# Kernel optimization log

Measured on AMD Instinct MI355X. Metric: run time of the kernel, lower is better.

The kernel has to match this reference:

```python
import jax, jax.numpy as jnp
import numpy as np
from jax import lax

WH = WW = 8          # window size
HEADS = 4

def _rel_index(Wh, Ww):
    # Swin-style static relative position index (N, N) with N = Wh*Ww
    coords = np.stack(np.meshgrid(np.arange(Wh), np.arange(Ww), indexing='ij')).reshape(2, -1)
    rel = coords[:, :, None] - coords[:, None, :]
    rel[0] += Wh - 1
    rel[1] += Ww - 1
    return jnp.asarray(rel[0] * (2 * Ww - 1) + rel[1], dtype=jnp.int32)

REL_IDX = _rel_index(WH, WW)  # (64, 64)

def _rep_pad1_detach(x):
    # ReplicationPad2dNaive(pad=1, detach=True): border copies carry no gradient
    xp = jnp.pad(lax.stop_gradient(x), ((0, 0), (0, 0), (1, 1), (1, 1)), mode='edge')
    return xp.at[:, :, 1:-1, 1:-1].set(x)

def setup_inputs() -> dict:
    key = jax.random.key(0)
    ks = jax.random.split(key, 6)
    B, C, H, W = 8, 192, 192, 192
    mid = 2 * C  # mlp_ratio=2
    s = 0.05
    return {
        'x': jax.random.normal(ks[0], (B, C, H, W), jnp.float32),
        'qkv_w': jax.random.normal(ks[1], (3 * C, C), jnp.float32) * s,
        'qkv_b': jnp.zeros((3 * C,), jnp.float32),
        'proj_w': jax.random.normal(ks[2], (C, C), jnp.float32) * s,
        'proj_b': jnp.zeros((C,), jnp.float32),
        'bias_table': jax.random.normal(ks[3], ((2 * WH - 1) * (2 * WW - 1),), jnp.float32) * s,
        'w1_w': jax.random.normal(ks[4], (mid, C), jnp.float32) * s,
        'w1_b': jnp.zeros((mid,), jnp.float32),
        'w2_w': jax.random.normal(ks[5], (C, mid // 2, 3, 3), jnp.float32) * s,
        'w2_b': jnp.zeros((C,), jnp.float32),
    }

def reference(x, qkv_w, qkv_b, proj_w, proj_b, bias_table, w1_w, w1_b, w2_w, w2_b):
    B, C, H, W = x.shape
    nh, nw = H // WH, W // WW
    N = WH * WW
    d = C // HEADS
    # ---- window partition: (B, C, H, W) -> (B*nWin, N, C) ----
    xw = x.reshape(B, C, nh, WH, nw, WW).transpose(0, 2, 4, 3, 5, 1).reshape(-1, N, C)
    # ---- qkv projection ----
    qkv = xw @ qkv_w.T + qkv_b                              # (Bn, N, 3C)
    qkv = qkv.reshape(-1, N, 3, HEADS, d).transpose(2, 0, 3, 1, 4)
    q, k, v = qkv[0], qkv[1], qkv[2]                        # (Bn, heads, N, d)
    # ---- attention with relative position bias ----
    bias = bias_table[REL_IDX]                              # (N, N)
    scores = jnp.einsum('bhnd,bhmd->bhnm', q, k) / jnp.sqrt(jnp.asarray(d, x.dtype))
    attn = jax.nn.softmax(scores + bias, axis=-1)
    out = jnp.einsum('bhnm,bhmd->bhnd', attn, v)            # (Bn, heads, N, d)
    out = out.transpose(0, 2, 1, 3).reshape(-1, N, C) @ proj_w.T + proj_b
    # ---- reverse window partition ----
    x1 = out.reshape(B, nh, nw, WH, WW, C).transpose(0, 5, 1, 3, 2, 4).reshape(B, C, H, W)
    x = x + x1
    # ---- GLU conv MLP residual branch ----
    h = jnp.einsum('bchw,oc->bohw', x, w1_w) + w1_b[:, None, None]  # 1x1 conv
    a, b = jnp.split(h, 2, axis=1)
    g = a * jax.nn.sigmoid(b)                               # GLU
    g = _rep_pad1_detach(g)
    y = lax.conv_general_dilated(g, w2_w, (1, 1), 'VALID',
                                 dimension_numbers=('NCHW', 'OIHW', 'NCHW'))
    y = y + w2_b[:, None, None]
    y = jnp.where(y >= 0, y, 0.2 * y)                       # leaky_relu(0.2)
    return x + y
```

## Files before the change

### kernel.cpp

```cpp
#include <hip/hip_runtime.h>
#include <hip/hip_bf16.h>

#define HWSZ (192*192)

typedef __attribute__((ext_vector_type(8))) short short8v;
typedef __attribute__((ext_vector_type(4))) float f32x4;

#define WG_N  331776
#define WQ2_N 110592
#define PW2_N 36864
#define W1_N  73728
#define WBYTES ((size_t)2*(WG_N+WQ2_N+PW2_N+W1_N))

__global__ __launch_bounds__(256)
void prep_weights(const float* __restrict__ w2_w, const float* __restrict__ qkv_w,
                  const float* __restrict__ proj_w, const float* __restrict__ w1_w,
                  __hip_bfloat16* __restrict__ wg, __hip_bfloat16* __restrict__ wq,
                  __hip_bfloat16* __restrict__ pw, __hip_bfloat16* __restrict__ w1b)
{
    int i = blockIdx.x*256 + threadIdx.x;
    if (i < WG_N) {
        int tap = i / 36864; int r = i - tap*36864;
        int oc = r / 192;    int c = r - oc*192;
        wg[i] = __float2bfloat16(w2_w[((size_t)oc*192 + c)*9 + tap]);
    } else if (i < WG_N + WQ2_N) {
        int j = i - WG_N;  wq[j] = __float2bfloat16(qkv_w[j]);
    } else if (i < WG_N + WQ2_N + PW2_N) {
        int j = i - WG_N - WQ2_N;  pw[j] = __float2bfloat16(proj_w[j]);
    } else if (i < WG_N + WQ2_N + PW2_N + W1_N) {
        int j = i - WG_N - WQ2_N - PW2_N;  w1b[j] = __float2bfloat16(w1_w[j]);
    }
}

__global__ __launch_bounds__(256, 2)
void wac_fused(const float* __restrict__ x,
               const __hip_bfloat16* __restrict__ wq, const float* __restrict__ qkv_b,
               const __hip_bfloat16* __restrict__ pw, const float* __restrict__ proj_b,
               const __hip_bfloat16* __restrict__ w1b, const float* __restrict__ w1_b,
               const float* __restrict__ bias_tab,
               __hip_bfloat16* __restrict__ g_ws, float* __restrict__ out)
{
    __shared__ __align__(16) __hip_bfloat16 Xs[64][200];
    __shared__ __align__(16) __hip_bfloat16 Os[64][200];
    __shared__ __align__(16) __hip_bfloat16 scr[4][2304];
    __shared__ __align__(16) __hip_bfloat16 bias_bf[64][66];

    const int tid = threadIdx.x;
    const int wid = (blockIdx.x & 7)*576 + (blockIdx.x >> 3);
    const int img = wid / 576;
    const int wr  = wid - img*576;
    const int wi  = wr / 24;
    const int wj  = wr - wi*24;

    const float* xb = x + (size_t)img*192*HWSZ + (size_t)(wi*8)*192 + wj*8;
    for (int i = tid; i < 12288; i += 256) {
        int c = i >> 6, t = i & 63;
        Xs[t][c] = __float2bfloat16(xb[(size_t)c*HWSZ + (t>>3)*192 + (t&7)]);
    }
    for (int i = tid; i < 4096; i += 256) {
        int tq = i >> 6, tk = i & 63;
        bias_bf[tq][tk] = __float2bfloat16(
            bias_tab[((tq>>3)-(tk>>3)+7)*15 + ((tq&7)-(tk&7)+7)]);
    }
    __syncthreads();

    const int lane = tid & 63;
    const int wv   = tid >> 6;
    const int lx   = lane & 15;
    const int kg   = lane >> 4;
    __hip_bfloat16* S = scr[wv];
    const short8v z8 = {0,0,0,0,0,0,0,0};
    const float scale = 0.14433756729740643f;

    short8v qAf[4][2], kBf[4][2], vBf[3][2];
    {
        f32x4 qa[9][4];
        #pragma unroll
        for (int j9=0;j9<9;j9++)
            #pragma unroll
            for (int n=0;n<4;n++) qa[j9][n] = (f32x4){0.f,0.f,0.f,0.f};

        #pragma unroll
        for (int kc=0; kc<6; ++kc) {
            short8v bfX[4];
            #pragma unroll
            for (int n=0;n<4;n++)
                bfX[n] = *(const short8v*)&Xs[n*16+lx][kc*32+kg*8];
            #pragma unroll
            for (int j9=0; j9<9; ++j9) {
                const int reg = j9/3, mm = j9 - reg*3;
                short8v af = *(const short8v*)
                    &wq[(size_t)(reg*192 + wv*48 + mm*16 + lx)*192 + kc*32 + kg*8];
                #pragma unroll
                for (int n=0;n<4;n++)
                    qa[j9][n] = __builtin_amdgcn_mfma_f32_16x16x32_bf16(
                                    af, bfX[n], qa[j9][n], 0,0,0);
            }
        }

        #pragma unroll
        for (int reg=0; reg<2; ++reg) {
            const int jrow0 = reg*192 + wv*48;
            float b4[3][4];
            #pragma unroll
            for (int mm=0;mm<3;mm++)
                #pragma unroll
                for (int r=0;r<4;r++) b4[mm][r] = qkv_b[jrow0 + mm*16 + kg*4 + r];
            #pragma unroll
            for (int hp=0; hp<2; ++hp) {
                #pragma unroll
                for (int mm=0;mm<3;mm++)
                    #pragma unroll
                    for (int nl=0;nl<2;nl++) {
                        union { ushort4 u; __hip_bfloat16 e[4]; } pk;
                        #pragma unroll
                        for (int r=0;r<4;r++)
                            pk.e[r] = __float2bfloat16(qa[reg*3+mm][hp*2+nl][r] + b4[mm][r]);
                        *(ushort4*)&S[(nl*16+lx)*56 + mm*16 + kg*4] = pk.u;
                    }
                #pragma unroll
                for (int mtl=0; mtl<2; ++mtl) {
                    short8v f0 = *(const short8v*)&S[(mtl*16+lx)*56 + kg*8];
                    short8v f1 = (kg<2) ? *(const short8v*)&S[(mtl*16+lx)*56 + 32 + kg*8] : z8;
                    if (reg==0) { qAf[hp*2+mtl][0]=f0; qAf[hp*2+mtl][1]=f1; }
                    else        { kBf[hp*2+mtl][0]=f0; kBf[hp*2+mtl][1]=f1; }
                }
            }
        }
        {
            const int jrow0 = 2*192 + wv*48;
            float b4[3][4];
            #pragma unroll
            for (int mm=0;mm<3;mm++)
                #pragma unroll
                for (int r=0;r<4;r++) b4[mm][r] = qkv_b[jrow0 + mm*16 + kg*4 + r];
            #pragma unroll
            for (int mm=0;mm<3;mm++) {
                #pragma unroll
                for (int n=0;n<4;n++)
                    #pragma unroll
                    for (int r=0;r<4;r++)
                        S[(kg*4+r)*72 + n*16+lx] =
                            __float2bfloat16(qa[6+mm][n][r] + b4[mm][r]);
                vBf[mm][0] = *(const short8v*)&S[lx*72 + kg*8];
                vBf[mm][1] = *(const short8v*)&S[lx*72 + 32 + kg*8];
            }
        }
    }

    f32x4 sa[4][4];
    #pragma unroll
    for (int m=0;m<4;m++)
        #pragma unroll
        for (int n=0;n<4;n++) sa[m][n] = (f32x4){0.f,0.f,0.f,0.f};
    #pragma unroll
    for (int kc2=0; kc2<2; ++kc2)
        #pragma unroll
        for (int m=0;m<4;m++)
            #pragma unroll
            for (int n=0;n<4;n++)
                sa[m][n] = __builtin_amdgcn_mfma_f32_16x16x32_bf16(
                               qAf[m][kc2], kBf[n][kc2], sa[m][n], 0,0,0);

    #pragma unroll
    for (int hp=0; hp<2; ++hp) {
        #pragma unroll
        for (int ml=0; ml<2; ++ml) {
            const int m = hp*2 + ml;
            #pragma unroll
            for (int r=0;r<4;r++) {
                const int trow = m*16 + kg*4 + r;
                float s[4];
                float mx = -1e30f;
                #pragma unroll
                for (int n=0;n<4;n++){
                    s[n] = sa[m][n][r]*scale + __bfloat162float(bias_bf[trow][n*16+lx]);
                    mx = fmaxf(mx, s[n]);
                }
                mx = fmaxf(mx, __shfl_xor(mx,1));
                mx = fmaxf(mx, __shfl_xor(mx,2));
                mx = fmaxf(mx, __shfl_xor(mx,4));
                mx = fmaxf(mx, __shfl_xor(mx,8));
                float l = 0.f;
                #pragma unroll
                for (int n=0;n<4;n++){ s[n] = __expf(s[n]-mx); l += s[n]; }
                l += __shfl_xor(l,1); l += __shfl_xor(l,2);
                l += __shfl_xor(l,4); l += __shfl_xor(l,8);
                const float inv = 1.f/l;
                #pragma unroll
                for (int n=0;n<4;n++)
                    S[(ml*16+kg*4+r)*72 + n*16+lx] = __float2bfloat16(s[n]*inv);
            }
        }
        short8v pA[2][2];
        #pragma unroll
        for (int ml=0; ml<2; ++ml) {
            pA[ml][0] = *(const short8v*)&S[(ml*16+lx)*72 + kg*8];
            pA[ml][1] = *(const short8v*)&S[(ml*16+lx)*72 + 32 + kg*8];
        }
        f32x4 oa[2][3];
        #pragma unroll
        for (int ml=0;ml<2;ml++)
            #pragma unroll
            for (int n=0;n<3;n++) oa[ml][n] = (f32x4){0.f,0.f,0.f,0.f};
        #pragma unroll
        for (int kc2=0; kc2<2; ++kc2)
            #pragma unroll
            for (int ml=0;ml<2;ml++)
                #pragma unroll
                for (int n=0;n<3;n++)
                    oa[ml][n] = __builtin_amdgcn_mfma_f32_16x16x32_bf16(
                                    pA[ml][kc2], vBf[n][kc2], oa[ml][n], 0,0,0);
        #pragma unroll
        for (int ml=0;ml<2;ml++)
            #pragma unroll
            for (int n=0;n<3;n++)
                #pragma unroll
                for (int r=0;r<4;r++)
                    Os[(hp*2+ml)*16+kg*4+r][wv*48 + n*16+lx] =
                        __float2bfloat16(oa[ml][n][r]);
    }
    __syncthreads();

    f32x4 pa[3][4];
    #pragma unroll
    for (int m=0;m<3;m++)
        #pragma unroll
        for (int n=0;n<4;n++) pa[m][n] = (f32x4){0.f,0.f,0.f,0.f};
    #pragma unroll
    for (int kc=0; kc<6; ++kc) {
        short8v bo[4];
        #pragma unroll
        for (int n=0;n<4;n++)
            bo[n] = *(const short8v*)&Os[n*16+lx][kc*32+kg*8];
        #pragma unroll
        for (int mm=0; mm<3; ++mm) {
            short8v ap = *(const short8v*)
                &pw[(size_t)(wv*48 + mm*16 + lx)*192 + kc*32 + kg*8];
            #pragma unroll
            for (int n=0;n<4;n++)
                pa[mm][n] = __builtin_amdgcn_mfma_f32_16x16x32_bf16(
                                ap, bo[n], pa[mm][n], 0,0,0);
        }
    }
    const size_t obase = (size_t)img*192*HWSZ + (size_t)(wi*8)*192 + wj*8;
    #pragma unroll
    for (int mm=0; mm<3; ++mm) {
        const int oc0 = wv*48 + mm*16 + kg*4;
        float pb4[4];
        #pragma unroll
        for (int r=0;r<4;r++) pb4[r] = proj_b[oc0+r];
        #pragma unroll
        for (int n=0;n<4;n++) {
            const int t = n*16 + lx;
            const size_t po = (size_t)(t>>3)*192 + (t&7);
            #pragma unroll
            for (int r=0;r<4;r++) {
                float v = pa[mm][n][r] + pb4[r] + __bfloat162float(Xs[t][oc0+r]);
                pa[mm][n][r] = v;
                out[obase + (size_t)(oc0+r)*HWSZ + po] = v;
            }
        }
    }
    __syncthreads();
    #pragma unroll
    for (int mm=0; mm<3; ++mm) {
        const int oc0 = wv*48 + mm*16 + kg*4;
        #pragma unroll
        for (int n=0;n<4;n++) {
            const int t = n*16 + lx;
            union { ushort4 u; __hip_bfloat16 e[4]; } pk;
            #pragma unroll
            for (int r=0;r<4;r++) pk.e[r] = __float2bfloat16(pa[mm][n][r]);
            *(ushort4*)&Os[t][oc0] = pk.u;
        }
    }
    __syncthreads();

    f32x4 ga[6][4];
    #pragma unroll
    for (int m=0;m<6;m++)
        #pragma unroll
        for (int n=0;n<4;n++) ga[m][n] = (f32x4){0.f,0.f,0.f,0.f};
    #pragma unroll
    for (int kc=0; kc<6; ++kc) {
        short8v bf2[4];
        #pragma unroll
        for (int n=0;n<4;n++)
            bf2[n] = *(const short8v*)&Os[n*16+lx][kc*32+kg*8];
        #pragma unroll
        for (int mm=0; mm<6; ++mm) {
            const int mrow = ((mm<3) ? (3*wv+mm) : (12 + 3*wv + mm-3))*16 + lx;
            short8v af = *(const short8v*)&w1b[(size_t)mrow*192 + kc*32 + kg*8];
            #pragma unroll
            for (int n=0;n<4;n++)
                ga[mm][n] = __builtin_amdgcn_mfma_f32_16x16x32_bf16(
                                af, bf2[n], ga[mm][n], 0,0,0);
        }
    }
    #pragma unroll
    for (int mm=0; mm<3; ++mm) {
        const int oc0 = (3*wv+mm)*16 + kg*4;
        float ba4[4], bb4[4];
        #pragma unroll
        for (int r=0;r<4;r++){ ba4[r] = w1_b[oc0+r]; bb4[r] = w1_b[oc0+r+192]; }
        #pragma unroll
        for (int n=0;n<4;n++) {
            union { ushort4 u; __hip_bfloat16 e[4]; } pk;
            #pragma unroll
            for (int r=0;r<4;r++) {
                const float a  = ga[mm][n][r]   + ba4[r];
                const float bv = ga[mm+3][n][r] + bb4[r];
                pk.e[r] = __float2bfloat16(a * (1.f/(1.f+__expf(-bv))));
            }
            *(ushort4*)&Xs[n*16+lx][oc0] = pk.u;
        }
    }
    __syncthreads();

    for (int i = tid; i < 1536; i += 256) {
        const int t = i / 24, c0 = (i - t*24)*8;
        const size_t ga_ = ((size_t)img*HWSZ +
                            (size_t)(wi*8 + (t>>3))*192 + wj*8 + (t&7))*192 + c0;
        *(uint4*)&g_ws[ga_] = *(const uint4*)&Xs[t][c0];
    }
}

#define KC 32
__global__ __launch_bounds__(512, 4)
void conv_mfma(const __hip_bfloat16* __restrict__ g,
               const __hip_bfloat16* __restrict__ wg,
               const float* __restrict__ w2_b, float* __restrict__ out, int img0)
{
    __shared__ __align__(16) __hip_bfloat16 gt[18*18*32];
    __shared__ __align__(16) __hip_bfloat16 wt[9*96*32];

    int bid = (blockIdx.x & 7)*288 + (blockIdx.x >> 3);
    const int tX = bid % 12; bid /= 12;
    const int tY = bid % 12; bid /= 12;
    const int ob = bid & 1;  bid >>= 1;
    const int bimg_l = bid;
    const int tx0 = tX*16, ty0 = tY*16, oc0 = ob*96;

    const int tid  = threadIdx.x;
    const int lane = tid & 63;
    const int wv   = tid >> 6;
    const int wm   = wv >> 2;
    const int wq   = wv & 3;
    const int lx   = lane & 15;
    const int kg   = lane >> 4;

    f32x4 acc[3][4];
    #pragma unroll
    for (int m=0;m<3;m++)
        #pragma unroll
        for (int n=0;n<4;n++) acc[m][n] = (f32x4){0.f,0.f,0.f,0.f};

    const size_t gbase = (size_t)bimg_l*HWSZ;

    for (int c0 = 0; c0 < 192; c0 += KC) {
        for (int idx = tid; idx < 1296; idx += 512) {
            int px = idx >> 2, part = idx & 3;
            int iy = px / 18, ix = px - iy*18;
            int gy = min(max(ty0 + iy - 1, 0), 191);
            int gx = min(max(tx0 + ix - 1, 0), 191);
            *(uint4*)&gt[(iy*18+ix)*32 + part*8] =
                *(const uint4*)&g[(gbase + (size_t)gy*192 + gx)*192 + c0 + part*8];
        }
        for (int idx = tid; idx < 3456; idx += 512) {
            int tap = idx / 384; int rr = idx - tap*384;
            int ocl = rr >> 2, part = rr & 3;
            *(uint4*)&wt[(tap*96+ocl)*32 + part*8] =
                *(const uint4*)&wg[(size_t)tap*36864 + (size_t)(oc0+ocl)*192 + c0 + part*8];
        }
        __syncthreads();

        #pragma unroll
        for (int kx=0; kx<3; ++kx) {
            short8v bb6[6];
            #pragma unroll
            for (int j=0;j<6;j++)
                bb6[j] = *(const short8v*)&gt[((wq*4 + j)*18 + lx + kx)*32 + kg*8];
            #pragma unroll
            for (int ky=0; ky<3; ++ky) {
                const int tap = ky*3+kx;
                short8v a[3];
                #pragma unroll
                for (int m=0;m<3;m++)
                    a[m] = *(const short8v*)&wt[(tap*96 + wm*48 + m*16 + lx)*32 + kg*8];
                #pragma unroll
                for (int m=0;m<3;m++)
                    #pragma unroll
                    for (int n=0;n<4;n++)
                        acc[m][n] = __builtin_amdgcn_mfma_f32_16x16x32_bf16(
                                        a[m], bb6[n+ky], acc[m][n], 0, 0, 0);
            }
        }
        __syncthreads();
    }

    #pragma unroll
    for (int m=0;m<3;m++) {
        const int ocb_ = oc0 + wm*48 + m*16 + kg*4;
        #pragma unroll
        for (int n=0;n<4;n++) {
            const int y = ty0 + wq*4 + n;
            const int xx = tx0 + lx;
            #pragma unroll
            for (int r=0;r<4;r++) {
                const int oc = ocb_ + r;
                const size_t o = ((size_t)((img0+bimg_l)*192+oc))*HWSZ + (size_t)y*192 + xx;
                float v = acc[m][n][r] + w2_b[oc];
                v = (v >= 0.f) ? v : 0.2f*v;
                out[o] += v;
            }
        }
    }
}

extern "C" void kernel_launch(void* const* d_in, const int* in_sizes, int n_in,
                              void* d_out, int out_size, void* d_ws, size_t ws_size,
                              hipStream_t stream)
{
    const float* x        = (const float*)d_in[0];
    const float* qkv_w    = (const float*)d_in[1];
    const float* qkv_b    = (const float*)d_in[2];
    const float* proj_w   = (const float*)d_in[3];
    const float* proj_b   = (const float*)d_in[4];
    const float* bias_tab = (const float*)d_in[5];
    const float* w1_w     = (const float*)d_in[6];
    const float* w1_b     = (const float*)d_in[7];
    const float* w2_w     = (const float*)d_in[8];
    const float* w2_b     = (const float*)d_in[9];
    float* out = (float*)d_out;

    char* base = (char*)d_ws;
    __hip_bfloat16* wg  = (__hip_bfloat16*)base;
    __hip_bfloat16* wqp = (__hip_bfloat16*)(base + (size_t)WG_N*2);
    __hip_bfloat16* pwp = (__hip_bfloat16*)(base + (size_t)(WG_N+WQ2_N)*2);
    __hip_bfloat16* w1b = (__hip_bfloat16*)(base + (size_t)(WG_N+WQ2_N+PW2_N)*2);
    __hip_bfloat16* g_ws = (__hip_bfloat16*)(base + WBYTES);

    prep_weights<<<2160, 256, 0, stream>>>(w2_w, qkv_w, proj_w, w1_w, wg, wqp, pwp, w1b);
    wac_fused   <<<4608, 256, 0, stream>>>(x, wqp, qkv_b, pwp, proj_b, w1b, w1_b,
                                           bias_tab, g_ws, out);
    conv_mfma   <<<2304, 512, 0, stream>>>(g_ws, wg, w2_b, out, 0);
}
```

Baseline: 672.6 us.

## Reuse Os as per-wave scratch and compute bias on the fly for 3 blocks/CU

Removes the per-wave scratch buffer and the 64x64 bf16 bias matrix from shared memory. Scratch traffic is redirected into each wave's 48-column slice of Os, and the relative position bias is gathered from a 225-entry float table at softmax time. The launch bound is raised to 3 blocks per CU so the smaller LDS footprint can buy occupancy. The new score-matrix layout in Os must not race with later uses of Os. The tighter register cap from the higher launch bound could cause spills.

After: 947.2 us. 1.41x slower.

```diff
diff --git a/kernel.cpp b/kernel.cpp
--- a/kernel.cpp
+++ b/kernel.cpp
@@ -32,7 +32,7 @@
     }
 }
 
-__global__ __launch_bounds__(256, 2)
+__global__ __launch_bounds__(256, 3)
 void wac_fused(const float* __restrict__ x,
                const __hip_bfloat16* __restrict__ wq, const float* __restrict__ qkv_b,
                const __hip_bfloat16* __restrict__ pw, const float* __restrict__ proj_b,
@@ -42,8 +42,7 @@
 {
     __shared__ __align__(16) __hip_bfloat16 Xs[64][200];
     __shared__ __align__(16) __hip_bfloat16 Os[64][200];
-    __shared__ __align__(16) __hip_bfloat16 scr[4][2304];
-    __shared__ __align__(16) __hip_bfloat16 bias_bf[64][66];
+    __shared__ float bias_f[225];
 
     const int tid = threadIdx.x;
     const int wid = (blockIdx.x & 7)*576 + (blockIdx.x >> 3);
@@ -57,18 +56,14 @@
         int c = i >> 6, t = i & 63;
         Xs[t][c] = __float2bfloat16(xb[(size_t)c*HWSZ + (t>>3)*192 + (t&7)]);
     }
-    for (int i = tid; i < 4096; i += 256) {
-        int tq = i >> 6, tk = i & 63;
-        bias_bf[tq][tk] = __float2bfloat16(
-            bias_tab[((tq>>3)-(tk>>3)+7)*15 + ((tq&7)-(tk&7)+7)]);
-    }
+    if (tid < 225) bias_f[tid] = bias_tab[tid];
     __syncthreads();
 
     const int lane = tid & 63;
     const int wv   = tid >> 6;
     const int lx   = lane & 15;
     const int kg   = lane >> 4;
-    __hip_bfloat16* S = scr[wv];
+    const int cb   = wv*48;
     const short8v z8 = {0,0,0,0,0,0,0,0};
     const float scale = 0.14433756729740643f;
 
@@ -116,12 +111,12 @@
                         #pragma unroll
                         for (int r=0;r<4;r++)
                             pk.e[r] = __float2bfloat16(qa[reg*3+mm][hp*2+nl][r] + b4[mm][r]);
-                        *(ushort4*)&S[(nl*16+lx)*56 + mm*16 + kg*4] = pk.u;
+                        *(ushort4*)&Os[nl*16+lx][cb + mm*16 + kg*4] = pk.u;
                     }
                 #pragma unroll
                 for (int mtl=0; mtl<2; ++mtl) {
-                    short8v f0 = *(const short8v*)&S[(mtl*16+lx)*56 + kg*8];
-                    short8v f1 = (kg<2) ? *(const short8v*)&S[(mtl*16+lx)*56 + 32 + kg*8] : z8;
+                    short8v f0 = *(const short8v*)&Os[mtl*16+lx][cb + kg*8];
+                    short8v f1 = (kg<2) ? *(const short8v*)&Os[mtl*16+lx][cb + 32 + kg*8] : z8;
                     if (reg==0) { qAf[hp*2+mtl][0]=f0; qAf[hp*2+mtl][1]=f1; }
                     else        { kBf[hp*2+mtl][0]=f0; kBf[hp*2+mtl][1]=f1; }
                 }
@@ -140,10 +135,10 @@
                 for (int n=0;n<4;n++)
                     #pragma unroll
                     for (int r=0;r<4;r++)
-                        S[(kg*4+r)*72 + n*16+lx] =
+                        Os[kg*4+r + 16*(n>>1)][cb + (n&1)*16 + lx] =
                             __float2bfloat16(qa[6+mm][n][r] + b4[mm][r]);
-                vBf[mm][0] = *(const short8v*)&S[lx*72 + kg*8];
-                vBf[mm][1] = *(const short8v*)&S[lx*72 + 32 + kg*8];
+                vBf[mm][0] = *(const short8v*)&Os[lx][cb + kg*8];
+                vBf[mm][1] = *(const short8v*)&Os[16+lx][cb + kg*8];
             }
         }
     }
@@ -164,17 +159,21 @@
 
     #pragma unroll
     for (int hp=0; hp<2; ++hp) {
+        short8v pA[2][2];
         #pragma unroll
         for (int ml=0; ml<2; ++ml) {
             const int m = hp*2 + ml;
             #pragma unroll
             for (int r=0;r<4;r++) {
                 const int trow = m*16 + kg*4 + r;
+                const int ty_ = trow>>3, tx_ = trow&7;
                 float s[4];
                 float mx = -1e30f;
                 #pragma unroll
                 for (int n=0;n<4;n++){
-                    s[n] = sa[m][n][r]*scale + __bfloat162float(bias_bf[trow][n*16+lx]);
+                    const int tk = n*16 + lx;
+                    s[n] = sa[m][n][r]*scale +
+                           bias_f[(ty_-(tk>>3)+7)*15 + (tx_-(tk&7)+7)];
                     mx = fmaxf(mx, s[n]);
                 }
                 mx = fmaxf(mx, __shfl_xor(mx,1));
@@ -189,14 +188,11 @@
                 const float inv = 1.f/l;
                 #pragma unroll
                 for (int n=0;n<4;n++)
-                    S[(ml*16+kg*4+r)*72 + n*16+lx] = __float2bfloat16(s[n]*inv);
-            }
-        }
-        short8v pA[2][2];
-        #pragma unroll
-        for (int ml=0; ml<2; ++ml) {
-            pA[ml][0] = *(const short8v*)&S[(ml*16+lx)*72 + kg*8];
-            pA[ml][1] = *(const short8v*)&S[(ml*16+lx)*72 + 32 + kg*8];
+                    Os[32 + kg*4+r + 16*(n>>1)][cb + (n&1)*16 + lx] =
+                        __float2bfloat16(s[n]*inv);
+            }
+            pA[ml][0] = *(const short8v*)&Os[32+lx][cb + kg*8];
+            pA[ml][1] = *(const short8v*)&Os[48+lx][cb + kg*8];
         }
         f32x4 oa[2][3];
         #pragma unroll
```
